# Kernel optimization log

Hardware: AMD Instinct MI355X
Metric: run time of the kernel (lower is better)

## Reference

```python
import jax, jax.numpy as jnp
import numpy as np

D_MODEL = 512
N_HEADS = 8
HEAD_DIM = D_MODEL // N_HEADS
ROPE_BASE = 10000.0


def _rope_cache(seq_len, dtype):
    half = HEAD_DIM // 2
    inv_freq = 1.0 / (ROPE_BASE ** (jnp.arange(half, dtype=dtype) / half))
    t = jnp.arange(seq_len, dtype=dtype)
    freqs = jnp.einsum('i,j->ij', t, inv_freq)            # [L, half]
    cos = jnp.repeat(jnp.cos(freqs), 2, axis=-1)          # [L, head_dim]
    sin = jnp.repeat(jnp.sin(freqs), 2, axis=-1)
    return cos[None, None], sin[None, None]               # [1,1,L,head_dim]


def _rotate_half(x):
    x_even = x[..., ::2]
    x_odd = x[..., 1::2]
    return jnp.stack([-x_odd, x_even], axis=-1).reshape(x.shape)


def setup_inputs() -> dict:
    key = jax.random.key(0)
    ks = jax.random.split(key, 10)
    B, Lq, Lkv, C = 2, 2048, 4096, D_MODEL
    s = 1.0 / np.sqrt(C)
    inp = {
        'q': jax.random.normal(ks[0], (B, Lq, C), jnp.float32),
        'kv': jax.random.normal(ks[1], (B, Lkv, C), jnp.float32),
        'Wq': jax.random.normal(ks[2], (C, C), jnp.float32) * s,
        'bq': jnp.zeros((C,), jnp.float32),
        'Wk': jax.random.normal(ks[3], (C, C), jnp.float32) * s,
        'bk': jnp.zeros((C,), jnp.float32),
        'Wv': jax.random.normal(ks[4], (C, C), jnp.float32) * s,
        'bv': jnp.zeros((C,), jnp.float32),
        'Wo': jax.random.normal(ks[5], (C, C), jnp.float32) * s,
        'bo': jnp.zeros((C,), jnp.float32),
    }
    return inp


def reference(q, kv, Wq, bq, Wk, bk, Wv, bv, Wo, bo):
    B, Lq, C = q.shape
    Lkv = kv.shape[1]
    H, Dh = N_HEADS, HEAD_DIM
    # projections (torch Linear: x @ W.T + b)
    qh = (q @ Wq.T + bq).reshape(B, Lq, H, Dh).transpose(0, 2, 1, 3)    # [B,H,Lq,Dh]
    kh = (kv @ Wk.T + bk).reshape(B, Lkv, H, Dh).transpose(0, 2, 1, 3)  # [B,H,Lkv,Dh]
    vh = (kv @ Wv.T + bv).reshape(B, Lkv, H, Dh).transpose(0, 2, 1, 3)
    # RoPE applied to K only
    cos, sin = _rope_cache(Lkv, kh.dtype)
    kh = kh * cos + _rotate_half(kh) * sin
    # manual softmax attention (full [B,H,Lq,Lkv] matrix, as in the source)
    scale = 1.0 / np.sqrt(Dh).astype(np.float32)
    attn = jnp.einsum('bhqd,bhkd->bhqk', qh, kh) * scale
    attn = jax.nn.softmax(attn, axis=-1)
    out = jnp.einsum('bhqk,bhkd->bhqd', attn, vh)
    out = out.transpose(0, 2, 1, 3).reshape(B, Lq, C)
    return out @ Wo.T + bo
```

## Files before the change

kernel.cpp:

```cpp
#include <hip/hip_runtime.h>
#include <math.h>

typedef _Float16 f16;
typedef __attribute__((ext_vector_type(8))) f16 f16x8;
typedef __attribute__((ext_vector_type(4))) float f32x4;
typedef __attribute__((ext_vector_type(4))) int   i32x4;

__device__ __forceinline__ short f2h(float f) {
    return __builtin_bit_cast(short, (f16)f);
}
__device__ __forceinline__ float h2f(short s) {
    return (float)__builtin_bit_cast(f16, s);
}

__device__ __forceinline__ void gload16(const void* g, void* l) {
    __builtin_amdgcn_global_load_lds(
        (const __attribute__((address_space(1))) unsigned int*)g,
        (__attribute__((address_space(3))) unsigned int*)l, 16, 0, 0);
}

#define MFMA16(A, B, C) __builtin_amdgcn_mfma_f32_16x16x32_f16(A, B, C, 0, 0, 0)
#define EXP2(x) __builtin_amdgcn_exp2f(x)

__global__ __launch_bounds__(256) void convert_kernel(
    const float* __restrict__ q, const float* __restrict__ kv,
    const float* __restrict__ Wq, const float* __restrict__ Wk,
    const float* __restrict__ Wv, const float* __restrict__ Wo,
    short* __restrict__ cq, short* __restrict__ ckv,
    short* __restrict__ wq, short* __restrict__ wk,
    short* __restrict__ wv, short* __restrict__ wo)
{
    int g = blockIdx.x * 256 + threadIdx.x;
    const float* src; short* dst; int local;
    if      (g <  524288) { src = q;  dst = cq;  local = g; }
    else if (g < 1572864) { src = kv; dst = ckv; local = g -  524288; }
    else if (g < 1638400) { src = Wq; dst = wq;  local = g - 1572864; }
    else if (g < 1703936) { src = Wk; dst = wk;  local = g - 1638400; }
    else if (g < 1769472) { src = Wv; dst = wv;  local = g - 1703936; }
    else                  { src = Wo; dst = wo;  local = g - 1769472; }
    float4 v = *(const float4*)(src + (size_t)local * 4);
    short4 hv; short* hp = (short*)&hv;
    hp[0] = f2h(v.x); hp[1] = f2h(v.y); hp[2] = f2h(v.z); hp[3] = f2h(v.w);
    *(short4*)(dst + (size_t)local * 4) = hv;
}

template<int RT, int EP>
__device__ __forceinline__ void gemm_core(
    short* As, short* Bs,
    const short* __restrict__ X, const short* __restrict__ W,
    const float* __restrict__ bias, float scale,
    float* __restrict__ outF, short* __restrict__ outH,
    int m0, int n0)
{
    const int tid  = threadIdx.x;
    const int wave = tid >> 6, lane = tid & 63;
    const int quad = lane >> 4, col = lane & 15;
    const int wy = wave >> 1, wx = wave & 1;
    constexpr int MT  = RT / 32;
    constexpr int ASZ = RT * 32;

    f32x4 acc[MT][4];
    #pragma unroll
    for (int i = 0; i < MT; ++i)
        #pragma unroll
        for (int j = 0; j < 4; ++j) acc[i][j] = (f32x4){0.f, 0.f, 0.f, 0.f};

    int aoff[MT], boff[4];
    #pragma unroll
    for (int t = 0; t < MT; ++t)
        aoff[t] = (wy * (RT / 2) + t * 16 + col) * 32 + quad * 8;
    #pragma unroll
    for (int t = 0; t < 4; ++t)
        boff[t] = (wx * 64 + t * 16 + col) * 32 + quad * 8;

    const short* Abase = X + (size_t)m0 * 512;
    const short* Bbase = W + (size_t)n0 * 512;

#define STAGE_G(BUF, KB) {                                                   \
    _Pragma("unroll")                                                        \
    for (int i = 0; i < RT / 64; ++i) {                                      \
        int p = i * 256 + tid; int r = p >> 2, qq = p & 3;                   \
        gload16(Abase + (size_t)r * 512 + (KB) + qq * 8,                     \
                &As[(BUF) * ASZ + (i * 256 + wave * 64) * 8]);               \
    }                                                                        \
    _Pragma("unroll")                                                        \
    for (int i = 0; i < 2; ++i) {                                            \
        int p = i * 256 + tid; int r = p >> 2, qq = p & 3;                   \
        gload16(Bbase + (size_t)r * 512 + (KB) + qq * 8,                     \
                &Bs[(BUF) * 4096 + (i * 256 + wave * 64) * 8]);              \
    }                                                                        \
}

    STAGE_G(0, 0);
    asm volatile("s_waitcnt vmcnt(0)" ::: "memory");
    __syncthreads();

    for (int kb = 0; kb < 512; kb += 32) {
        const int cur = (kb >> 5) & 1;
        if (kb + 32 < 512) STAGE_G(cur ^ 1, kb + 32);
        f16x8 a[MT], b[4];
        #pragma unroll
        for (int t = 0; t < MT; ++t) a[t] = *(const f16x8*)&As[cur * ASZ + aoff[t]];
        #pragma unroll
        for (int t = 0; t < 4; ++t)  b[t] = *(const f16x8*)&Bs[cur * 4096 + boff[t]];
        #pragma unroll
        for (int tm = 0; tm < MT; ++tm)
            #pragma unroll
            for (int tn = 0; tn < 4; ++tn)
                acc[tm][tn] = MFMA16(a[tm], b[tn], acc[tm][tn]);
        asm volatile("s_waitcnt vmcnt(0)" ::: "memory");
        __syncthreads();
    }
#undef STAGE_G

    #pragma unroll
    for (int tn = 0; tn < 4; ++tn) {
        int ng = n0 + wx * 64 + tn * 16 + col;
        float bb = bias[ng];
        #pragma unroll
        for (int tm = 0; tm < MT; ++tm) {
            int mb = m0 + wy * (RT / 2) + tm * 16 + quad * 4;
            if constexpr (EP == 2) {
                int bb_ = mb >> 12, kvg = mb & 4095;
                int tile = kvg >> 7, kv128 = kvg & 127;
                int t01 = (kv128 >> 6) & 1, sv = (kv128 >> 4) & 3, qd = (kv128 >> 2) & 3;
                int hh = ng >> 6, dd = ng & 63, dt = dd >> 4, d15 = dd & 15;
                size_t base = ((((size_t)((bb_ * 8 + hh) * 32 + tile) * 16)
                               + sv * 4 + dt) * 64 + qd * 16 + d15) * 8 + t01 * 4;
                short4 s4; short* sp = (short*)&s4;
                #pragma unroll
                for (int r = 0; r < 4; ++r) sp[r] = f2h(acc[tm][tn][r] + bb);
                *(short4*)&outH[base] = s4;
            } else if constexpr (EP == 1) {
                #pragma unroll
                for (int r = 0; r < 4; ++r)
                    outH[(size_t)(mb + r) * 512 + ng] =
                        f2h((acc[tm][tn][r] + bb) * scale);
            } else {
                #pragma unroll
                for (int r = 0; r < 4; ++r)
                    outF[(size_t)(mb + r) * 512 + ng] = acc[tm][tn][r] + bb;
            }
        }
    }
}

__global__ __launch_bounds__(256) void fused_qkv_gemm_kernel(
    const short* __restrict__ cq, const short* __restrict__ ckv,
    const short* __restrict__ wq, const short* __restrict__ wk,
    const short* __restrict__ wv,
    const float* __restrict__ bq, const float* __restrict__ bk,
    const float* __restrict__ bv, float qscale,
    short* __restrict__ Qh, short* __restrict__ Kh, short* __restrict__ Vf)
{
    __shared__ short As[2 * 128 * 32], Bs[2 * 128 * 32];
    int bi = blockIdx.x;
    if (bi < 128) {
        gemm_core<128, 1>(As, Bs, cq, wq, bq, qscale, nullptr, Qh,
                          (bi >> 2) * 128, (bi & 3) * 128);
    } else if (bi < 384) {
        bi -= 128;
        gemm_core<128, 1>(As, Bs, ckv, wk, bk, 1.0f, nullptr, Kh,
                          (bi >> 2) * 128, (bi & 3) * 128);
    } else {
        bi -= 384;
        gemm_core<128, 2>(As, Bs, ckv, wv, bv, 1.0f, nullptr, Vf,
                          (bi >> 2) * 128, (bi & 3) * 128);
    }
}

__global__ __launch_bounds__(256) void gemm_o_kernel(
    const short* __restrict__ X, const short* __restrict__ W,
    const float* __restrict__ bias, float* __restrict__ outF)
{
    __shared__ short As[2 * 64 * 32], Bs[2 * 128 * 32];
    gemm_core<64, 0>(As, Bs, X, W, bias, 1.0f, outF, nullptr,
                     (int)(blockIdx.x >> 2) * 64, (int)(blockIdx.x & 3) * 128);
}

__global__ __launch_bounds__(256) void rope_kernel(short* __restrict__ Kh)
{
    __shared__ float2 tbl[4][32];
    const int t = threadIdx.x;
    const int g = blockIdx.x * 256 + t;
    if (t < 128) {
        int p = t >> 5, i = t & 31;
        int pos = (blockIdx.x * 4 + p) & 4095;
        float fr = expf((float)i * -0.28782313662425576f);
        float sv, cv;
        sincosf((float)pos * fr, &sv, &cv);
        tbl[p][i] = make_float2(cv, sv);
    }
    __syncthreads();

    int row = g >> 6;
    int c8  = (g & 63) * 8;
    size_t off = (size_t)row * 512 + c8;
    f16x8 hv = *(const f16x8*)&Kh[off];
    float x[8];
    #pragma unroll
    for (int j = 0; j < 8; ++j) x[j] = (float)hv[j];
    const int rl = row & 3;
    const int ib = (c8 & 63) >> 1;
    #pragma unroll
    for (int p = 0; p < 4; ++p) {
        float2 cs = tbl[rl][ib + p];
        float e = x[2 * p], o = x[2 * p + 1];
        x[2 * p]     = e * cs.x - o * cs.y;
        x[2 * p + 1] = o * cs.x + e * cs.y;
    }
    #pragma unroll
    for (int j = 0; j < 8; ++j) hv[j] = (f16)x[j];
    *(f16x8*)&Kh[off] = hv;
}

__global__ __launch_bounds__(256, 2) void attn_mfma_kernel(
    const short* __restrict__ Qh, const short* __restrict__ Kh,
    const short* __restrict__ Vfrag, short* __restrict__ AO)
{
    __shared__ char smem[34816];

    const int tid  = threadIdx.x;
    const int wave = tid >> 6;
    const int lane = tid & 63;
    const int quad = lane >> 4;
    const int l15  = lane & 15;

    const int bh = blockIdx.x & 15;
    const int qt = blockIdx.x >> 4;
    const int b  = bh >> 3, h = bh & 7;
    const int qb = qt * 64;

    f16x8 qf[4][2];
    #pragma unroll
    for (int tq = 0; tq < 4; ++tq)
        #pragma unroll
        for (int c = 0; c < 2; ++c)
            qf[tq][c] = *(const f16x8*)&Qh[((size_t)(b * 2048 + qb + tq * 16 + l15)) * 512
                                           + h * 64 + c * 32 + quad * 8];

    f32x4 o[4][4];
    f32x4 l4[4];
    #pragma unroll
    for (int i = 0; i < 4; ++i) {
        l4[i] = (f32x4){0.f, 0.f, 0.f, 0.f};
        #pragma unroll
        for (int j = 0; j < 4; ++j) o[i][j] = (f32x4){0.f, 0.f, 0.f, 0.f};
    }

    const f32x4 zero4 = (f32x4){0.f, 0.f, 0.f, 0.f};
    f16x8 vones;
    #pragma unroll
    for (int j = 0; j < 8; ++j) vones[j] = (f16)1.0f;

    const short* kp = Kh + ((size_t)(b * 4096 + wave * 16 + l15)) * 512
                      + h * 64 + quad * 8;
    const short* vbase = Vfrag + (size_t)(b * 8 + h) * 262144
                         + ((size_t)(wave * 4) * 64 + lane) * 8;

#define LDK(DST, I) { const short* _k = kp + (size_t)(I) * 65536;            \
    DST[0] = *(const f16x8*)(_k);                                            \
    DST[1] = *(const f16x8*)(_k + 32);                                       \
    DST[2] = *(const f16x8*)(_k + 32768);                                    \
    DST[3] = *(const f16x8*)(_k + 32800); }
#define LDV(DST, I) { const short* _v = vbase + (size_t)(I) * 8192;          \
    DST[0] = *(const f16x8*)(_v);                                            \
    DST[1] = *(const f16x8*)(_v + 512);                                      \
    DST[2] = *(const f16x8*)(_v + 1024);                                     \
    DST[3] = *(const f16x8*)(_v + 1536); }

#define QK(KC) {                                                             \
    __builtin_amdgcn_s_setprio(1);                                           \
    _Pragma("unroll")                                                        \
    for (int t = 0; t < 4; ++t) {                                            \
        s0[t] = MFMA16(KC[0], qf[t][0], zero4);                              \
        s0[t] = MFMA16(KC[1], qf[t][1], s0[t]);                              \
        s1[t] = MFMA16(KC[2], qf[t][0], zero4);                              \
        s1[t] = MFMA16(KC[3], qf[t][1], s1[t]);                              \
    }                                                                        \
    __builtin_amdgcn_s_setprio(0); }

#define FIN(VP) {                                                            \
    _Pragma("unroll")                                                        \
    for (int t = 0; t < 4; ++t) {                                            \
        float e0 = EXP2(s0[t][0]), e1 = EXP2(s0[t][1]);                      \
        float e2 = EXP2(s0[t][2]), e3 = EXP2(s0[t][3]);                      \
        float e4 = EXP2(s1[t][0]), e5 = EXP2(s1[t][1]);                      \
        float e6 = EXP2(s1[t][2]), e7 = EXP2(s1[t][3]);                      \
        i32x4 pw;                                                            \
        pw.x = __builtin_bit_cast(int, __builtin_amdgcn_cvt_pkrtz(e0, e1));  \
        pw.y = __builtin_bit_cast(int, __builtin_amdgcn_cvt_pkrtz(e2, e3));  \
        pw.z = __builtin_bit_cast(int, __builtin_amdgcn_cvt_pkrtz(e4, e5));  \
        pw.w = __builtin_bit_cast(int, __builtin_amdgcn_cvt_pkrtz(e6, e7));  \
        f16x8 p8 = __builtin_bit_cast(f16x8, pw);                            \
        __builtin_amdgcn_s_setprio(1);                                       \
        _Pragma("unroll")                                                    \
        for (int dt = 0; dt < 4; ++dt)                                       \
            o[t][dt] = MFMA16(p8, VP[dt], o[t][dt]);                         \
        l4[t] = MFMA16(p8, vones, l4[t]);                                    \
        __builtin_amdgcn_s_setprio(0);                                       \
    } }

#define BODY(I, KC, KN, VP) {                                                \
    LDK(KN, (I) + 1);                                                        \
    FIN(VP);                                                                 \
    LDV(VP, (I) + 1);                                                        \
    QK(KC); }

    f16x8 kA[4], kB[4], vA[4], vB[4];
    f32x4 s0[4], s1[4];

    LDK(kA, 0); LDV(vA, 0); LDK(kB, 1); LDV(vB, 1);
    QK(kA);

    #pragma unroll 1
    for (int j = 1; j < 31; j += 2) {
        BODY(j,     kB, kA, vA);
        BODY(j + 1, kA, kB, vB);
    }
    BODY(31, kB, kA, vA);
    FIN(vB);

#undef BODY
#undef FIN
#undef QK
#undef LDV
#undef LDK

    float* Opart = (float*)smem;
    float* Lpart = (float*)(smem + 33792);

    float inv_save[8];
    #pragma unroll
    for (int pass = 0; pass < 2; ++pass) {
        if (pass) __syncthreads();
        #pragma unroll
        for (int tq = 0; tq < 4; ++tq)
            #pragma unroll
            for (int dh = 0; dh < 2; ++dh) {
                int dt = pass * 2 + dh;
                #pragma unroll
                for (int r = 0; r < 4; ++r)
                    Opart[wave * (64 * 33) + (tq * 16 + quad * 4 + r) * 33 + dh * 16 + l15] = o[tq][dt][r];
            }
        if (pass == 0 && l15 == 0) {
            #pragma unroll
            for (int tq = 0; tq < 4; ++tq)
                #pragma unroll
                for (int r = 0; r < 4; ++r)
                    Lpart[wave * 64 + tq * 16 + quad * 4 + r] = l4[tq][r];
        }
        __syncthreads();
        #pragma unroll
        for (int r = 0; r < 8; ++r) {
            int qq = wave * 16 + r * 2 + (lane >> 5);
            int d  = lane & 31;
            float v = Opart[0 * (64 * 33) + qq * 33 + d] + Opart[1 * (64 * 33) + qq * 33 + d]
                    + Opart[2 * (64 * 33) + qq * 33 + d] + Opart[3 * (64 * 33) + qq * 33 + d];
            float inv;
            if (pass == 0) {
                float l = Lpart[qq] + Lpart[64 + qq] + Lpart[128 + qq] + Lpart[192 + qq];
                inv = 1.0f / l;
                inv_save[r] = inv;
            } else {
                inv = inv_save[r];
            }
            float val = v * inv;
            size_t oo = ((size_t)(b * 2048 + qb + qq)) * 512 + h * 64 + pass * 32 + d;
            AO[oo] = f2h(val);
        }
    }
}

extern "C" void kernel_launch(void* const* d_in, const int* in_sizes, int n_in,
                              void* d_out, int out_size, void* d_ws, size_t ws_size,
                              hipStream_t stream) {
    const float* q  = (const float*)d_in[0];
    const float* kv = (const float*)d_in[1];
    const float* Wq = (const float*)d_in[2];
    const float* bq = (const float*)d_in[3];
    const float* Wk = (const float*)d_in[4];
    const float* bk = (const float*)d_in[5];
    const float* Wv = (const float*)d_in[6];
    const float* bv = (const float*)d_in[7];
    const float* Wo = (const float*)d_in[8];
    const float* bo = (const float*)d_in[9];
    float* out = (float*)d_out;

    char* ws = (char*)d_ws;
    const size_t MB = 1024 * 1024;
    short* cq  = (short*)(ws + 0 * MB);
    short* ckv = (short*)(ws + 4 * MB);
    short* wq  = (short*)(ws + 12 * MB);
    short* wk  = wq + 262144;
    short* wv  = wk + 262144;
    short* wo  = wv + 262144;
    short* Qh  = (short*)(ws + 14 * MB);
    short* Kh  = (short*)(ws + 18 * MB);
    short* Vf  = (short*)(ws + 26 * MB);
    short* AO  = (short*)(ws + 34 * MB);

    const float qscale = 0.18033688011112043f;

    dim3 blk(256);
    convert_kernel<<<7168, blk, 0, stream>>>(
        q, kv, Wq, Wk, Wv, Wo, cq, ckv, wq, wk, wv, wo);

    fused_qkv_gemm_kernel<<<640, blk, 0, stream>>>(
        cq, ckv, wq, wk, wv, bq, bk, bv, qscale, Qh, Kh, Vf);

    rope_kernel<<<2048, blk, 0, stream>>>(Kh);

    attn_mfma_kernel<<<512, blk, 0, stream>>>(Qh, Kh, Vf, AO);

    gemm_o_kernel<<<256, blk, 0, stream>>>(AO, wo, bo, out);
}
```

Measured before the change: 166.1 us.

## Halve attention query tile, drop K double-buffer, deepen GEMM k-step to 64

```diff
diff --git a/kernel.cpp b/kernel.cpp
--- a/kernel.cpp
+++ b/kernel.cpp
@@ -8,9 +8,6 @@
 
 __device__ __forceinline__ short f2h(float f) {
     return __builtin_bit_cast(short, (f16)f);
-}
-__device__ __forceinline__ float h2f(short s) {
-    return (float)__builtin_bit_cast(f16, s);
 }
 
 __device__ __forceinline__ void gload16(const void* g, void* l) {
@@ -57,7 +54,7 @@
     const int quad = lane >> 4, col = lane & 15;
     const int wy = wave >> 1, wx = wave & 1;
     constexpr int MT  = RT / 32;
-    constexpr int ASZ = RT * 32;
+    constexpr int ASZ = RT * 64;
 
     f32x4 acc[MT][4];
     #pragma unroll
@@ -68,26 +65,26 @@
     int aoff[MT], boff[4];
     #pragma unroll
     for (int t = 0; t < MT; ++t)
-        aoff[t] = (wy * (RT / 2) + t * 16 + col) * 32 + quad * 8;
+        aoff[t] = (wy * (RT / 2) + t * 16 + col) * 64 + quad * 8;
     #pragma unroll
     for (int t = 0; t < 4; ++t)
-        boff[t] = (wx * 64 + t * 16 + col) * 32 + quad * 8;
+        boff[t] = (wx * 64 + t * 16 + col) * 64 + quad * 8;
 
     const short* Abase = X + (size_t)m0 * 512;
     const short* Bbase = W + (size_t)n0 * 512;
 
 #define STAGE_G(BUF, KB) {                                                   \
     _Pragma("unroll")                                                        \
-    for (int i = 0; i < RT / 64; ++i) {                                      \
-        int p = i * 256 + tid; int r = p >> 2, qq = p & 3;                   \
+    for (int i = 0; i < RT / 32; ++i) {                                      \
+        int p = i * 256 + tid; int r = p >> 3, qq = p & 7;                   \
         gload16(Abase + (size_t)r * 512 + (KB) + qq * 8,                     \
                 &As[(BUF) * ASZ + (i * 256 + wave * 64) * 8]);               \
     }                                                                        \
     _Pragma("unroll")                                                        \
-    for (int i = 0; i < 2; ++i) {                                            \
-        int p = i * 256 + tid; int r = p >> 2, qq = p & 3;                   \
+    for (int i = 0; i < 4; ++i) {                                            \
+        int p = i * 256 + tid; int r = p >> 3, qq = p & 7;                   \
         gload16(Bbase + (size_t)r * 512 + (KB) + qq * 8,                     \
-                &Bs[(BUF) * 4096 + (i * 256 + wave * 64) * 8]);              \
+                &Bs[(BUF) * 8192 + (i * 256 + wave * 64) * 8]);              \
     }                                                                        \
 }
 
@@ -95,19 +92,27 @@
     asm volatile("s_waitcnt vmcnt(0)" ::: "memory");
     __syncthreads();
 
-    for (int kb = 0; kb < 512; kb += 32) {
-        const int cur = (kb >> 5) & 1;
-        if (kb + 32 < 512) STAGE_G(cur ^ 1, kb + 32);
-        f16x8 a[MT], b[4];
-        #pragma unroll
-        for (int t = 0; t < MT; ++t) a[t] = *(const f16x8*)&As[cur * ASZ + aoff[t]];
-        #pragma unroll
-        for (int t = 0; t < 4; ++t)  b[t] = *(const f16x8*)&Bs[cur * 4096 + boff[t]];
-        #pragma unroll
-        for (int tm = 0; tm < MT; ++tm)
+    for (int kb = 0; kb < 512; kb += 64) {
+        const int cur = (kb >> 6) & 1;
+        if (kb + 64 < 512) STAGE_G(cur ^ 1, kb + 64);
+        f16x8 a[MT][2], b[4][2];
+        #pragma unroll
+        for (int t = 0; t < MT; ++t)
             #pragma unroll
-            for (int tn = 0; tn < 4; ++tn)
-                acc[tm][tn] = MFMA16(a[tm], b[tn], acc[tm][tn]);
+            for (int ks = 0; ks < 2; ++ks)
+                a[t][ks] = *(const f16x8*)&As[cur * ASZ + aoff[t] + ks * 32];
+        #pragma unroll
+        for (int t = 0; t < 4; ++t)
+            #pragma unroll
+            for (int ks = 0; ks < 2; ++ks)
+                b[t][ks] = *(const f16x8*)&Bs[cur * 8192 + boff[t] + ks * 32];
+        #pragma unroll
+        for (int ks = 0; ks < 2; ++ks)
+            #pragma unroll
+            for (int tm = 0; tm < MT; ++tm)
+                #pragma unroll
+                for (int tn = 0; tn < 4; ++tn)
+                    acc[tm][tn] = MFMA16(a[tm][ks], b[tn][ks], acc[tm][tn]);
         asm volatile("s_waitcnt vmcnt(0)" ::: "memory");
         __syncthreads();
     }
@@ -153,7 +158,7 @@
     const float* __restrict__ bv, float qscale,
     short* __restrict__ Qh, short* __restrict__ Kh, short* __restrict__ Vf)
 {
-    __shared__ short As[2 * 128 * 32], Bs[2 * 128 * 32];
+    __shared__ short As[2 * 128 * 64], Bs[2 * 128 * 64];
     int bi = blockIdx.x;
     if (bi < 128) {
         gemm_core<128, 1>(As, Bs, cq, wq, bq, qscale, nullptr, Qh,
@@ -173,7 +178,7 @@
     const short* __restrict__ X, const short* __restrict__ W,
     const float* __restrict__ bias, float* __restrict__ outF)
 {
-    __shared__ short As[2 * 64 * 32], Bs[2 * 128 * 32];
+    __shared__ short As[2 * 64 * 64], Bs[2 * 128 * 64];
     gemm_core<64, 0>(As, Bs, X, W, bias, 1.0f, outF, nullptr,
                      (int)(blockIdx.x >> 2) * 64, (int)(blockIdx.x & 3) * 128);
 }
@@ -214,11 +219,11 @@
     *(f16x8*)&Kh[off] = hv;
 }
 
-__global__ __launch_bounds__(256, 2) void attn_mfma_kernel(
+__global__ __launch_bounds__(256, 3) void attn_mfma_kernel(
     const short* __restrict__ Qh, const short* __restrict__ Kh,
     const short* __restrict__ Vfrag, short* __restrict__ AO)
 {
-    __shared__ char smem[34816];
+    __shared__ char smem[17408];
 
     const int tid  = threadIdx.x;
     const int wave = tid >> 6;
@@ -229,20 +234,20 @@
     const int bh = blockIdx.x & 15;
     const int qt = blockIdx.x >> 4;
     const int b  = bh >> 3, h = bh & 7;
-    const int qb = qt * 64;
-
-    f16x8 qf[4][2];
-    #pragma unroll
-    for (int tq = 0; tq < 4; ++tq)
+    const int qb = qt * 32;
+
+    f16x8 qf[2][2];
+    #pragma unroll
+    for (int tq = 0; tq < 2; ++tq)
         #pragma unroll
         for (int c = 0; c < 2; ++c)
             qf[tq][c] = *(const f16x8*)&Qh[((size_t)(b * 2048 + qb + tq * 16 + l15)) * 512
                                            + h * 64 + c * 32 + quad * 8];
 
-    f32x4 o[4][4];
-    f32x4 l4[4];
-    #pragma unroll
-    for (int i = 0; i < 4; ++i) {
+    f32x4 o[2][4];
+    f32x4 l4[2];
+    #pragma unroll
+    for (int i = 0; i < 2; ++i) {
         l4[i] = (f32x4){0.f, 0.f, 0.f, 0.f};
         #pragma unroll
         for (int j = 0; j < 4; ++j) o[i][j] = (f32x4){0.f, 0.f, 0.f, 0.f};
@@ -272,7 +277,7 @@
 #define QK(KC) {                                                             \
     __builtin_amdgcn_s_setprio(1);                                           \
     _Pragma("unroll")                                                        \
-    for (int t = 0; t < 4; ++t) {                                            \
+    for (int t = 0; t < 2; ++t) {                                            \
         s0[t] = MFMA16(KC[0], qf[t][0], zero4);                              \
         s0[t] = MFMA16(KC[1], qf[t][1], s0[t]);                              \
         s1[t] = MFMA16(KC[2], qf[t][0], zero4);                              \
@@ -282,7 +287,7 @@
 
 #define FIN(VP) {                                                            \
     _Pragma("unroll")                                                        \
-    for (int t = 0; t < 4; ++t) {                                            \
+    for (int t = 0; t < 2; ++t) {                                            \
         float e0 = EXP2(s0[t][0]), e1 = EXP2(s0[t][1]);                      \
         float e2 = EXP2(s0[t][2]), e3 = EXP2(s0[t][3]);                      \
         float e4 = EXP2(s1[t][0]), e5 = EXP2(s1[t][1]);                      \
@@ -301,24 +306,26 @@
         __builtin_amdgcn_s_setprio(0);                                       \
     } }
 
-#define BODY(I, KC, KN, VP) {                                                \
-    LDK(KN, (I) + 1);                                                        \
+#define BODY(I, VP) {                                                        \
+    LDK(kK, (I));                                                            \
     FIN(VP);                                                                 \
     LDV(VP, (I) + 1);                                                        \
-    QK(KC); }
-
-    f16x8 kA[4], kB[4], vA[4], vB[4];
-    f32x4 s0[4], s1[4];
-
-    LDK(kA, 0); LDV(vA, 0); LDK(kB, 1); LDV(vB, 1);
-    QK(kA);
+    QK(kK); }
+
+    f16x8 kK[4], vA[4], vB[4];
+    f32x4 s0[2], s1[2];
+
+    LDV(vA, 0);
+    LDK(kK, 0);
+    LDV(vB, 1);
+    QK(kK);
 
     #pragma unroll 1
     for (int j = 1; j < 31; j += 2) {
-        BODY(j,     kB, kA, vA);
-        BODY(j + 1, kA, kB, vB);
-    }
-    BODY(31, kB, kA, vA);
+        BODY(j,     vA);
+        BODY(j + 1, vB);
+    }
+    BODY(31, vA);
     FIN(vB);
 
 #undef BODY
@@ -328,38 +335,38 @@
 #undef LDK
 
     float* Opart = (float*)smem;
-    float* Lpart = (float*)(smem + 33792);
-
-    float inv_save[8];
+    float* Lpart = (float*)(smem + 16896);
+
+    float inv_save[4];
     #pragma unroll
     for (int pass = 0; pass < 2; ++pass) {
         if (pass) __syncthreads();
         #pragma unroll
-        for (int tq = 0; tq < 4; ++tq)
+        for (int tq = 0; tq < 2; ++tq)
             #pragma unroll
             for (int dh = 0; dh < 2; ++dh) {
                 int dt = pass * 2 + dh;
                 #pragma unroll
                 for (int r = 0; r < 4; ++r)
-                    Opart[wave * (64 * 33) + (tq * 16 + quad * 4 + r) * 33 + dh * 16 + l15] = o[tq][dt][r];
+                    Opart[wave * (32 * 33) + (tq * 16 + quad * 4 + r) * 33 + dh * 16 + l15] = o[tq][dt][r];
             }
         if (pass == 0 && l15 == 0) {
             #pragma unroll
-            for (int tq = 0; tq < 4; ++tq)
+            for (int tq = 0; tq < 2; ++tq)
                 #pragma unroll
                 for (int r = 0; r < 4; ++r)
-                    Lpart[wave * 64 + tq * 16 + quad * 4 + r] = l4[tq][r];
+                    Lpart[wave * 32 + tq * 16 + quad * 4 + r] = l4[tq][r];
         }
         __syncthreads();
         #pragma unroll
-        for (int r = 0; r < 8; ++r) {
-            int qq = wave * 16 + r * 2 + (lane >> 5);
+        for (int r = 0; r < 4; ++r) {
+            int qq = wave * 8 + r * 2 + (lane >> 5);
             int d  = lane & 31;
-            float v = Opart[0 * (64 * 33) + qq * 33 + d] + Opart[1 * (64 * 33) + qq * 33 + d]
-                    + Opart[2 * (64 * 33) + qq * 33 + d] + Opart[3 * (64 * 33) + qq * 33 + d];
+            float v = Opart[0 * (32 * 33) + qq * 33 + d] + Opart[1 * (32 * 33) + qq * 33 + d]
+                    + Opart[2 * (32 * 33) + qq * 33 + d] + Opart[3 * (32 * 33) + qq * 33 + d];
             float inv;
             if (pass == 0) {
-                float l = Lpart[qq] + Lpart[64 + qq] + Lpart[128 + qq] + Lpart[192 + qq];
+                float l = Lpart[qq] + Lpart[32 + qq] + Lpart[64 + qq] + Lpart[96 + qq];
                 inv = 1.0f / l;
                 inv_save[r] = inv;
             } else {
@@ -411,7 +418,7 @@
 
     rope_kernel<<<2048, blk, 0, stream>>>(Kh);
 
-    attn_mfma_kernel<<<512, blk, 0, stream>>>(Qh, Kh, Vf, AO);
+    attn_mfma_kernel<<<1024, blk, 0, stream>>>(Qh, Kh, Vf, AO);
 
     gemm_o_kernel<<<256, blk, 0, stream>>>(AO, wo, bo, out);
 }
```

Result: slower. 209.2 us (+26.0%).

## Split attention KV range across 8 waves and sum row totals on VALU

Applied to the files above, without the earlier changes.

```diff
diff --git a/kernel.cpp b/kernel.cpp
--- a/kernel.cpp
+++ b/kernel.cpp
@@ -8,9 +8,6 @@
 
 __device__ __forceinline__ short f2h(float f) {
     return __builtin_bit_cast(short, (f16)f);
-}
-__device__ __forceinline__ float h2f(short s) {
-    return (float)__builtin_bit_cast(f16, s);
 }
 
 __device__ __forceinline__ void gload16(const void* g, void* l) {
@@ -214,14 +211,16 @@
     *(f16x8*)&Kh[off] = hv;
 }
 
-__global__ __launch_bounds__(256, 2) void attn_mfma_kernel(
+__global__ __launch_bounds__(512, 2) void attn_mfma_kernel(
     const short* __restrict__ Qh, const short* __restrict__ Kh,
     const short* __restrict__ Vfrag, short* __restrict__ AO)
 {
-    __shared__ char smem[34816];
+    __shared__ char smem[36864];
 
     const int tid  = threadIdx.x;
     const int wave = tid >> 6;
+    const int w4   = wave & 3;
+    const int wt   = wave >> 2;
     const int lane = tid & 63;
     const int quad = lane >> 4;
     const int l15  = lane & 15;
@@ -240,30 +239,25 @@
                                            + h * 64 + c * 32 + quad * 8];
 
     f32x4 o[4][4];
-    f32x4 l4[4];
-    #pragma unroll
-    for (int i = 0; i < 4; ++i) {
-        l4[i] = (f32x4){0.f, 0.f, 0.f, 0.f};
+    float lsum[4] = {0.f, 0.f, 0.f, 0.f};
+    #pragma unroll
+    for (int i = 0; i < 4; ++i)
         #pragma unroll
         for (int j = 0; j < 4; ++j) o[i][j] = (f32x4){0.f, 0.f, 0.f, 0.f};
-    }
 
     const f32x4 zero4 = (f32x4){0.f, 0.f, 0.f, 0.f};
-    f16x8 vones;
-    #pragma unroll
-    for (int j = 0; j < 8; ++j) vones[j] = (f16)1.0f;
-
-    const short* kp = Kh + ((size_t)(b * 4096 + wave * 16 + l15)) * 512
+
+    const short* kp = Kh + ((size_t)(b * 4096 + wt * 128 + w4 * 16 + l15)) * 512
                       + h * 64 + quad * 8;
-    const short* vbase = Vfrag + (size_t)(b * 8 + h) * 262144
-                         + ((size_t)(wave * 4) * 64 + lane) * 8;
-
-#define LDK(DST, I) { const short* _k = kp + (size_t)(I) * 65536;            \
+    const short* vbase = Vfrag + (size_t)(b * 8 + h) * 262144 + (size_t)wt * 8192
+                         + ((size_t)(w4 * 4) * 64 + lane) * 8;
+
+#define LDK(DST, I) { const short* _k = kp + (size_t)(I) * 131072;           \
     DST[0] = *(const f16x8*)(_k);                                            \
     DST[1] = *(const f16x8*)(_k + 32);                                       \
     DST[2] = *(const f16x8*)(_k + 32768);                                    \
     DST[3] = *(const f16x8*)(_k + 32800); }
-#define LDV(DST, I) { const short* _v = vbase + (size_t)(I) * 8192;          \
+#define LDV(DST, I) { const short* _v = vbase + (size_t)(I) * 16384;         \
     DST[0] = *(const f16x8*)(_v);                                            \
     DST[1] = *(const f16x8*)(_v + 512);                                      \
     DST[2] = *(const f16x8*)(_v + 1024);                                     \
@@ -287,6 +281,7 @@
         float e2 = EXP2(s0[t][2]), e3 = EXP2(s0[t][3]);                      \
         float e4 = EXP2(s1[t][0]), e5 = EXP2(s1[t][1]);                      \
         float e6 = EXP2(s1[t][2]), e7 = EXP2(s1[t][3]);                      \
+        lsum[t] += ((e0 + e1) + (e2 + e3)) + ((e4 + e5) + (e6 + e7));        \
         i32x4 pw;                                                            \
         pw.x = __builtin_bit_cast(int, __builtin_amdgcn_cvt_pkrtz(e0, e1));  \
         pw.y = __builtin_bit_cast(int, __builtin_amdgcn_cvt_pkrtz(e2, e3));  \
@@ -297,7 +292,6 @@
         _Pragma("unroll")                                                    \
         for (int dt = 0; dt < 4; ++dt)                                       \
             o[t][dt] = MFMA16(p8, VP[dt], o[t][dt]);                         \
-        l4[t] = MFMA16(p8, vones, l4[t]);                                    \
         __builtin_amdgcn_s_setprio(0);                                       \
     } }
 
@@ -314,11 +308,11 @@
     QK(kA);
 
     #pragma unroll 1
-    for (int j = 1; j < 31; j += 2) {
+    for (int j = 1; j < 15; j += 2) {
         BODY(j,     kB, kA, vA);
         BODY(j + 1, kA, kB, vB);
     }
-    BODY(31, kB, kA, vA);
+    BODY(15, kB, kA, vA);
     FIN(vB);
 
 #undef BODY
@@ -327,47 +321,50 @@
 #undef LDV
 #undef LDK
 
+    #pragma unroll
+    for (int t = 0; t < 4; ++t) {
+        lsum[t] += __shfl_xor(lsum[t], 16);
+        lsum[t] += __shfl_xor(lsum[t], 32);
+    }
+
     float* Opart = (float*)smem;
-    float* Lpart = (float*)(smem + 33792);
-
-    float inv_save[8];
-    #pragma unroll
-    for (int pass = 0; pass < 2; ++pass) {
-        if (pass) __syncthreads();
+    float* Lpart = (float*)(smem + 34816);
+
+    const int d  = tid & 15;
+    const int qi = tid >> 4;
+    float inv_save[2];
+    #pragma unroll
+    for (int p = 0; p < 4; ++p) {
+        if (p) __syncthreads();
         #pragma unroll
         for (int tq = 0; tq < 4; ++tq)
             #pragma unroll
-            for (int dh = 0; dh < 2; ++dh) {
-                int dt = pass * 2 + dh;
-                #pragma unroll
-                for (int r = 0; r < 4; ++r)
-                    Opart[wave * (64 * 33) + (tq * 16 + quad * 4 + r) * 33 + dh * 16 + l15] = o[tq][dt][r];
-            }
-        if (pass == 0 && l15 == 0) {
+            for (int r = 0; r < 4; ++r)
+                Opart[wave * 1088 + (tq * 16 + quad * 4 + r) * 17 + l15] = o[tq][p][r];
+        if (p == 0 && quad == 0) {
             #pragma unroll
             for (int tq = 0; tq < 4; ++tq)
-                #pragma unroll
-                for (int r = 0; r < 4; ++r)
-                    Lpart[wave * 64 + tq * 16 + quad * 4 + r] = l4[tq][r];
+                Lpart[wave * 64 + tq * 16 + l15] = lsum[tq];
         }
         __syncthreads();
         #pragma unroll
-        for (int r = 0; r < 8; ++r) {
-            int qq = wave * 16 + r * 2 + (lane >> 5);
-            int d  = lane & 31;
-            float v = Opart[0 * (64 * 33) + qq * 33 + d] + Opart[1 * (64 * 33) + qq * 33 + d]
-                    + Opart[2 * (64 * 33) + qq * 33 + d] + Opart[3 * (64 * 33) + qq * 33 + d];
+        for (int hq = 0; hq < 2; ++hq) {
+            int qq = qi + hq * 32;
+            float v = 0.f;
+            #pragma unroll
+            for (int w = 0; w < 8; ++w) v += Opart[w * 1088 + qq * 17 + d];
             float inv;
-            if (pass == 0) {
-                float l = Lpart[qq] + Lpart[64 + qq] + Lpart[128 + qq] + Lpart[192 + qq];
+            if (p == 0) {
+                float l = 0.f;
+                #pragma unroll
+                for (int w = 0; w < 8; ++w) l += Lpart[w * 64 + qq];
                 inv = 1.0f / l;
-                inv_save[r] = inv;
+                inv_save[hq] = inv;
             } else {
-                inv = inv_save[r];
+                inv = inv_save[hq];
             }
-            float val = v * inv;
-            size_t oo = ((size_t)(b * 2048 + qb + qq)) * 512 + h * 64 + pass * 32 + d;
-            AO[oo] = f2h(val);
+            size_t oo = ((size_t)(b * 2048 + qb + qq)) * 512 + h * 64 + p * 16 + d;
+            AO[oo] = f2h(v * inv);
         }
     }
 }
@@ -411,7 +408,7 @@
 
     rope_kernel<<<2048, blk, 0, stream>>>(Kh);
 
-    attn_mfma_kernel<<<512, blk, 0, stream>>>(Qh, Kh, Vf, AO);
+    attn_mfma_kernel<<<512, dim3(512), 0, stream>>>(Qh, Kh, Vf, AO);
 
     gemm_o_kernel<<<256, blk, 0, stream>>>(AO, wo, bo, out);
 }
```

Result: slower. 223.6 us (+34.6%).

## Fuse RoPE into K projection epilogue and replace MFMA row-sum with scalar sums

Applied to the files above, without the earlier changes.

```diff
diff --git a/kernel.cpp b/kernel.cpp
--- a/kernel.cpp
+++ b/kernel.cpp
@@ -8,9 +8,6 @@
 
 __device__ __forceinline__ short f2h(float f) {
     return __builtin_bit_cast(short, (f16)f);
-}
-__device__ __forceinline__ float h2f(short s) {
-    return (float)__builtin_bit_cast(f16, s);
 }
 
 __device__ __forceinline__ void gload16(const void* g, void* l) {
@@ -28,9 +25,19 @@
     const float* __restrict__ Wv, const float* __restrict__ Wo,
     short* __restrict__ cq, short* __restrict__ ckv,
     short* __restrict__ wq, short* __restrict__ wk,
-    short* __restrict__ wv, short* __restrict__ wo)
+    short* __restrict__ wv, short* __restrict__ wo,
+    float2* __restrict__ rtbl)
 {
     int g = blockIdx.x * 256 + threadIdx.x;
+    if (g >= 1835008) {
+        int idx = g - 1835008;
+        int pos = idx >> 5, i = idx & 31;
+        float fr = expf((float)i * -0.28782313662425576f);
+        float sv, cv;
+        sincosf((float)pos * fr, &sv, &cv);
+        rtbl[idx] = make_float2(cv, sv);
+        return;
+    }
     const float* src; short* dst; int local;
     if      (g <  524288) { src = q;  dst = cq;  local = g; }
     else if (g < 1572864) { src = kv; dst = ckv; local = g -  524288; }
@@ -44,11 +51,12 @@
     *(short4*)(dst + (size_t)local * 4) = hv;
 }
 
-template<int RT, int EP>
+template<int RT, int EP, bool ROPE>
 __device__ __forceinline__ void gemm_core(
     short* As, short* Bs,
     const short* __restrict__ X, const short* __restrict__ W,
     const float* __restrict__ bias, float scale,
+    const float2* __restrict__ rtbl,
     float* __restrict__ outF, short* __restrict__ outH,
     int m0, int n0)
 {
@@ -133,9 +141,17 @@
                 *(short4*)&outH[base] = s4;
             } else if constexpr (EP == 1) {
                 #pragma unroll
-                for (int r = 0; r < 4; ++r)
-                    outH[(size_t)(mb + r) * 512 + ng] =
-                        f2h((acc[tm][tn][r] + bb) * scale);
+                for (int r = 0; r < 4; ++r) {
+                    float val = acc[tm][tn][r] + bb;
+                    if constexpr (ROPE) {
+                        float pr = __shfl_xor(val, 1);
+                        int pos = (mb + r) & 4095;
+                        float2 cs = rtbl[pos * 32 + ((ng & 63) >> 1)];
+                        val = (ng & 1) ? (val * cs.x + pr * cs.y)
+                                       : (val * cs.x - pr * cs.y);
+                    }
+                    outH[(size_t)(mb + r) * 512 + ng] = f2h(val * scale);
+                }
             } else {
                 #pragma unroll
                 for (int r = 0; r < 4; ++r)
@@ -151,21 +167,22 @@
     const short* __restrict__ wv,
     const float* __restrict__ bq, const float* __restrict__ bk,
     const float* __restrict__ bv, float qscale,
+    const float2* __restrict__ rtbl,
     short* __restrict__ Qh, short* __restrict__ Kh, short* __restrict__ Vf)
 {
     __shared__ short As[2 * 128 * 32], Bs[2 * 128 * 32];
     int bi = blockIdx.x;
     if (bi < 128) {
-        gemm_core<128, 1>(As, Bs, cq, wq, bq, qscale, nullptr, Qh,
-                          (bi >> 2) * 128, (bi & 3) * 128);
+        gemm_core<128, 1, false>(As, Bs, cq, wq, bq, qscale, nullptr, nullptr, Qh,
+                                 (bi >> 2) * 128, (bi & 3) * 128);
     } else if (bi < 384) {
         bi -= 128;
-        gemm_core<128, 1>(As, Bs, ckv, wk, bk, 1.0f, nullptr, Kh,
-                          (bi >> 2) * 128, (bi & 3) * 128);
+        gemm_core<128, 1, true>(As, Bs, ckv, wk, bk, 1.0f, rtbl, nullptr, Kh,
+                                (bi >> 2) * 128, (bi & 3) * 128);
     } else {
         bi -= 384;
-        gemm_core<128, 2>(As, Bs, ckv, wv, bv, 1.0f, nullptr, Vf,
-                          (bi >> 2) * 128, (bi & 3) * 128);
+        gemm_core<128, 2, false>(As, Bs, ckv, wv, bv, 1.0f, nullptr, nullptr, Vf,
+                                 (bi >> 2) * 128, (bi & 3) * 128);
     }
 }
 
@@ -174,44 +191,8 @@
     const float* __restrict__ bias, float* __restrict__ outF)
 {
     __shared__ short As[2 * 64 * 32], Bs[2 * 128 * 32];
-    gemm_core<64, 0>(As, Bs, X, W, bias, 1.0f, outF, nullptr,
-                     (int)(blockIdx.x >> 2) * 64, (int)(blockIdx.x & 3) * 128);
-}
-
-__global__ __launch_bounds__(256) void rope_kernel(short* __restrict__ Kh)
-{
-    __shared__ float2 tbl[4][32];
-    const int t = threadIdx.x;
-    const int g = blockIdx.x * 256 + t;
-    if (t < 128) {
-        int p = t >> 5, i = t & 31;
-        int pos = (blockIdx.x * 4 + p) & 4095;
-        float fr = expf((float)i * -0.28782313662425576f);
-        float sv, cv;
-        sincosf((float)pos * fr, &sv, &cv);
-        tbl[p][i] = make_float2(cv, sv);
-    }
-    __syncthreads();
-
-    int row = g >> 6;
-    int c8  = (g & 63) * 8;
-    size_t off = (size_t)row * 512 + c8;
-    f16x8 hv = *(const f16x8*)&Kh[off];
-    float x[8];
-    #pragma unroll
-    for (int j = 0; j < 8; ++j) x[j] = (float)hv[j];
-    const int rl = row & 3;
-    const int ib = (c8 & 63) >> 1;
-    #pragma unroll
-    for (int p = 0; p < 4; ++p) {
-        float2 cs = tbl[rl][ib + p];
-        float e = x[2 * p], o = x[2 * p + 1];
-        x[2 * p]     = e * cs.x - o * cs.y;
-        x[2 * p + 1] = o * cs.x + e * cs.y;
-    }
-    #pragma unroll
-    for (int j = 0; j < 8; ++j) hv[j] = (f16)x[j];
-    *(f16x8*)&Kh[off] = hv;
+    gemm_core<64, 0, false>(As, Bs, X, W, bias, 1.0f, nullptr, outF, nullptr,
+                            (int)(blockIdx.x >> 2) * 64, (int)(blockIdx.x & 3) * 128);
 }
 
 __global__ __launch_bounds__(256, 2) void attn_mfma_kernel(
@@ -240,18 +221,13 @@
                                            + h * 64 + c * 32 + quad * 8];
 
     f32x4 o[4][4];
-    f32x4 l4[4];
-    #pragma unroll
-    for (int i = 0; i < 4; ++i) {
-        l4[i] = (f32x4){0.f, 0.f, 0.f, 0.f};
+    float lsum[4] = {0.f, 0.f, 0.f, 0.f};
+    #pragma unroll
+    for (int i = 0; i < 4; ++i)
         #pragma unroll
         for (int j = 0; j < 4; ++j) o[i][j] = (f32x4){0.f, 0.f, 0.f, 0.f};
-    }
 
     const f32x4 zero4 = (f32x4){0.f, 0.f, 0.f, 0.f};
-    f16x8 vones;
-    #pragma unroll
-    for (int j = 0; j < 8; ++j) vones[j] = (f16)1.0f;
 
     const short* kp = Kh + ((size_t)(b * 4096 + wave * 16 + l15)) * 512
                       + h * 64 + quad * 8;
@@ -287,6 +263,7 @@
         float e2 = EXP2(s0[t][2]), e3 = EXP2(s0[t][3]);                      \
         float e4 = EXP2(s1[t][0]), e5 = EXP2(s1[t][1]);                      \
         float e6 = EXP2(s1[t][2]), e7 = EXP2(s1[t][3]);                      \
+        lsum[t] += ((e0 + e1) + (e2 + e3)) + ((e4 + e5) + (e6 + e7));        \
         i32x4 pw;                                                            \
         pw.x = __builtin_bit_cast(int, __builtin_amdgcn_cvt_pkrtz(e0, e1));  \
         pw.y = __builtin_bit_cast(int, __builtin_amdgcn_cvt_pkrtz(e2, e3));  \
@@ -297,7 +274,6 @@
         _Pragma("unroll")                                                    \
         for (int dt = 0; dt < 4; ++dt)                                       \
             o[t][dt] = MFMA16(p8, VP[dt], o[t][dt]);                         \
-        l4[t] = MFMA16(p8, vones, l4[t]);                                    \
         __builtin_amdgcn_s_setprio(0);                                       \
     } }
 
@@ -326,6 +302,12 @@
 #undef QK
 #undef LDV
 #undef LDK
+
+    #pragma unroll
+    for (int t = 0; t < 4; ++t) {
+        lsum[t] += __shfl_xor(lsum[t], 16);
+        lsum[t] += __shfl_xor(lsum[t], 32);
+    }
 
     float* Opart = (float*)smem;
     float* Lpart = (float*)(smem + 33792);
@@ -343,12 +325,10 @@
                 for (int r = 0; r < 4; ++r)
                     Opart[wave * (64 * 33) + (tq * 16 + quad * 4 + r) * 33 + dh * 16 + l15] = o[tq][dt][r];
             }
-        if (pass == 0 && l15 == 0) {
+        if (pass == 0 && quad == 0) {
             #pragma unroll
             for (int tq = 0; tq < 4; ++tq)
-                #pragma unroll
-                for (int r = 0; r < 4; ++r)
-                    Lpart[wave * 64 + tq * 16 + quad * 4 + r] = l4[tq][r];
+                Lpart[wave * 64 + tq * 16 + l15] = lsum[tq];
         }
         __syncthreads();
         #pragma unroll
@@ -399,17 +379,16 @@
     short* Kh  = (short*)(ws + 18 * MB);
     short* Vf  = (short*)(ws + 26 * MB);
     short* AO  = (short*)(ws + 34 * MB);
+    float2* rtbl = (float2*)(ws + 38 * MB);
 
     const float qscale = 0.18033688011112043f;
 
     dim3 blk(256);
-    convert_kernel<<<7168, blk, 0, stream>>>(
-        q, kv, Wq, Wk, Wv, Wo, cq, ckv, wq, wk, wv, wo);
+    convert_kernel<<<7680, blk, 0, stream>>>(
+        q, kv, Wq, Wk, Wv, Wo, cq, ckv, wq, wk, wv, wo, rtbl);
 
     fused_qkv_gemm_kernel<<<640, blk, 0, stream>>>(
-        cq, ckv, wq, wk, wv, bq, bk, bv, qscale, Qh, Kh, Vf);
-
-    rope_kernel<<<2048, blk, 0, stream>>>(Kh);
+        cq, ckv, wq, wk, wv, bq, bk, bv, qscale, rtbl, Qh, Kh, Vf);
 
     attn_mfma_kernel<<<512, blk, 0, stream>>>(Qh, Kh, Vf, AO);
 
```

Result: slower. 229.2 us (+38.0%).
